# Optimization experiments

Hardware: AMD Instinct MI355X
Metric: run time of the kernel (lower is better)

Reference implementation:

```python
import jax, jax.numpy as jnp
import numpy as np

EPS = 1e-6

def setup_inputs() -> dict:
    key = jax.random.key(0)
    ks = jax.random.split(key, 8)
    B, L, Dm, N, K = 2, 1024, 1024, 64, 4
    Di = Dm * 2  # expand=2
    g = lambda k, shape, scale: jax.random.normal(k, shape, jnp.float32) * scale
    return {
        "x": g(ks[0], (B, L, Dm), 1.0),
        "norm_w": jnp.ones((Dm,), jnp.float32),
        "in_proj_w": g(ks[1], (2 * Di, Dm), 0.02),
        "conv_w": g(ks[2], (Di, 1, K), 0.1),      # depthwise: [out=Di, in/groups=1, K]
        "conv_b": jnp.zeros((Di,), jnp.float32),
        "x_proj_w": g(ks[3], (2 * N, Di), 0.02),
        "dt_w": g(ks[4], (Di, Di), 0.02),
        "dt_b": jnp.ones((Di,), jnp.float32),      # init.constant_(dt_proj.bias, 1.0)
        "A_log": g(ks[5], (Di, N), 1.0) - 4.0,     # normal(mean=-4, std=1)
        "D_param": jnp.ones((Di,), jnp.float32),
        "out_proj_w": g(ks[6], (Dm, Di), 0.02),
    }

def reference(x, norm_w, in_proj_w, conv_w, conv_b, x_proj_w, dt_w, dt_b, A_log, D_param, out_proj_w):
    B, L, Dm = x.shape
    Di = conv_w.shape[0]
    K = conv_w.shape[-1]
    skip = x
    # RMSNorm
    rms = jnp.sqrt(jnp.mean(x * x, axis=-1, keepdims=True) + EPS)
    xn = norm_w * (x / rms)
    # in_proj -> [B,L,2*Di], split into x and res
    xr = xn @ in_proj_w.T
    xi, res = jnp.split(xr, 2, axis=-1)
    # causal depthwise conv1d (pad left K-1, truncate to L == torch pad=K-1 then [:L])
    xc = jax.lax.conv_general_dilated(
        xi.transpose(0, 2, 1), conv_w, window_strides=(1,),
        padding=[(K - 1, 0)], dimension_numbers=("NCH", "OIH", "NCH"),
        feature_group_count=Di)
    xc = (xc + conv_b[None, :, None]).transpose(0, 2, 1)  # [B,L,Di]
    xc = jax.nn.silu(xc)
    # selective scan
    x_dbl = xc @ x_proj_w.T                   # [B,L,2N]; first half (delta) unused, as in source
    _delta, B_ssm = jnp.split(x_dbl, 2, axis=-1)  # B_ssm: [B,L,N]
    dt = jax.nn.softplus(xc @ dt_w.T + dt_b)  # [B,L,Di]
    A = -jnp.exp(A_log.astype(jnp.float32))   # [Di,N]
    N = A.shape[-1]

    def step(h, inp):
        x_t, dt_t, B_t = inp                   # [B,Di],[B,Di],[B,N]
        A_disc = jnp.exp(A[None, :, :] * dt_t[:, :, None])   # [B,Di,N]
        h = A_disc * h + B_t[:, None, :] * x_t[:, :, None]   # [B,Di,N]
        y_t = h.sum(axis=-1) + D_param * x_t                 # [B,Di]
        return h, y_t

    h0 = jnp.zeros((B, Di, N), xc.dtype)
    _, ys = jax.lax.scan(step, h0, (xc.transpose(1, 0, 2), dt.transpose(1, 0, 2), B_ssm.transpose(1, 0, 2)))
    y = ys.transpose(1, 0, 2)                  # [B,L,Di]
    out = (y * jax.nn.silu(res)) @ out_proj_w.T
    return out + skip
```

## Files before the change

kernel.cpp:

```cpp
#include <hip/hip_runtime.h>
#include <hip/hip_bf16.h>
#include <math.h>

#define L_DIM 1024
#define DM 1024
#define DI 2048
#define NS 64

typedef __attribute__((ext_vector_type(8))) short short8;
typedef __attribute__((ext_vector_type(4))) float f32x4;

__device__ __forceinline__ ushort bf16u(float f)
{
    unsigned u = __float_as_uint(f);
    unsigned r = (u + 0x7fffu + ((u >> 16) & 1u)) >> 16;
    return (ushort)r;
}
__device__ __forceinline__ float bf2f(ushort u)
{
    return __uint_as_float((unsigned)u << 16);
}

__device__ __forceinline__ void gld16(const ushort* g, const ushort* l)
{
    __builtin_amdgcn_global_load_lds(
        (const __attribute__((address_space(1))) unsigned int*)g,
        (__attribute__((address_space(3))) unsigned int*)l, 16, 0, 0);
}

__global__ __launch_bounds__(256) void k_rms_xn(const float* __restrict__ x,
    const float* __restrict__ nw, ushort* __restrict__ d)
{
    int row = blockIdx.x;
    const float* xp = x + (size_t)row * DM;
    float4 v = ((const float4*)xp)[threadIdx.x];
    float ss = v.x*v.x + v.y*v.y + v.z*v.z + v.w*v.w;
    #pragma unroll
    for (int m = 32; m; m >>= 1) ss += __shfl_xor(ss, m, 64);
    __shared__ float red[4];
    if ((threadIdx.x & 63) == 0) red[threadIdx.x >> 6] = ss;
    __syncthreads();
    float tot = red[0] + red[1] + red[2] + red[3];
    float ri = rsqrtf(tot * (1.0f / DM) + 1e-6f);
    float4 wv = ((const float4*)nw)[threadIdx.x];
    ((ushort4*)(d + (size_t)row * DM))[threadIdx.x] =
        make_ushort4(bf16u(v.x*ri*wv.x), bf16u(v.y*ri*wv.y),
                     bf16u(v.z*ri*wv.z), bf16u(v.w*ri*wv.w));
}

__device__ __forceinline__ void cast8(const float* __restrict__ s,
                                      ushort* __restrict__ d, int i)
{
    float4 a = ((const float4*)s)[2*i], b = ((const float4*)s)[2*i+1];
    ((ushort4*)d)[2*i]   = make_ushort4(bf16u(a.x), bf16u(a.y), bf16u(a.z), bf16u(a.w));
    ((ushort4*)d)[2*i+1] = make_ushort4(bf16u(b.x), bf16u(b.y), bf16u(b.z), bf16u(b.w));
}
__global__ __launch_bounds__(256) void k_castw(
    const float* __restrict__ s0, ushort* __restrict__ d0,
    const float* __restrict__ s1, ushort* __restrict__ d1,
    const float* __restrict__ s2, ushort* __restrict__ d2,
    const float* __restrict__ s3, ushort* __restrict__ d3)
{
    int i = blockIdx.x * 256 + threadIdx.x;
    if (i < 524288)       cast8(s0, d0, i);
    else if (i < 1048576) cast8(s1, d1, i - 524288);
    else if (i < 1064960) cast8(s2, d2, i - 1048576);
    else                  cast8(s3, d3, i - 1064960);
}

template<int MODE, int BM>
__global__ __launch_bounds__(256) void k_mfma(
    const ushort* __restrict__ Abf, const ushort* __restrict__ Bbf0,
    const ushort* __restrict__ Bbf1, float* __restrict__ C0,
    ushort* __restrict__ C0b, float* __restrict__ C1,
    const float* __restrict__ bias, const float* __restrict__ skip,
    int Kdim, int ldc)
{
    constexpr int NI = (BM == 128) ? 4 : 2;
    constexpr int SA = BM / 32;
    __shared__ __align__(16) ushort As[BM*64];
    __shared__ __align__(16) ushort Bs[128*64];
    const int t = threadIdx.x, w = t >> 6, lane = t & 63;
    const int nwg = gridDim.x * gridDim.y;
    const int orig = blockIdx.y * gridDim.x + blockIdx.x;
    const int swz = (orig & 7) * (nwg >> 3) + (orig >> 3);
    const int nt = swz % gridDim.x, mt = swz / gridDim.x;
    const int mBase = mt * BM, nBase = nt * 128;
    const bool isXP = (MODE == 1) && (nt == 16);
    const ushort* __restrict__ Bbf = isXP ? Bbf1 : Bbf0;
    const int wr = (BM == 128) ? (w >> 1) * 64 : 0;
    const int wc = (BM == 128) ? (w & 1) * 64 : w * 32;
    const int sR = lane >> 3;
    const int sK = ((lane & 7) ^ sR) * 8;

    f32x4 acc[4][NI];
    #pragma unroll
    for (int i = 0; i < 4; ++i)
        #pragma unroll
        for (int j = 0; j < NI; ++j)
            acc[i][j] = (f32x4){0.f, 0.f, 0.f, 0.f};

    for (int kt = 0; kt < Kdim; kt += 64) {
        #pragma unroll
        for (int s = 0; s < SA; ++s) {
            int tr = w*8 + s*32 + sR;
            gld16(Abf + (size_t)(mBase + tr) * Kdim + kt + sK,
                  As + (w*8 + s*32) * 64);
        }
        #pragma unroll
        for (int s = 0; s < 4; ++s) {
            int tr = w*8 + s*32 + sR;
            int gr = isXP ? (tr < 63 ? tr : 63) : (nBase + tr);
            gld16(Bbf + (size_t)gr * Kdim + kt + sK,
                  Bs + (w*8 + s*32) * 64);
        }
        __syncthreads();
        #pragma unroll
        for (int kk = 0; kk < 2; ++kk) {
            short8 af[4], bfr[NI];
            #pragma unroll
            for (int f = 0; f < 4; ++f) {
                int ra = wr + f*16 + (lane & 15);
                int ca = (kk*4 + (lane >> 4)) ^ (ra & 7);
                af[f] = *(const short8*)(As + ra*64 + ca*8);
            }
            #pragma unroll
            for (int f = 0; f < NI; ++f) {
                int rb2 = wc + f*16 + (lane & 15);
                int cb2 = (kk*4 + (lane >> 4)) ^ (rb2 & 7);
                bfr[f] = *(const short8*)(Bs + rb2*64 + cb2*8);
            }
            #pragma unroll
            for (int mi = 0; mi < 4; ++mi)
                #pragma unroll
                for (int ni = 0; ni < NI; ++ni)
                    acc[mi][ni] = __builtin_amdgcn_mfma_f32_16x16x32_bf16(
                        af[mi], bfr[ni], acc[mi][ni], 0, 0, 0);
        }
        __syncthreads();
    }

    const int rb = (lane >> 4) * 4, cbl = lane & 15;
    #pragma unroll
    for (int mi = 0; mi < 4; ++mi) {
        #pragma unroll
        for (int ni = 0; ni < NI; ++ni) {
            int ltcol = wc + ni*16 + cbl;
            int col = nBase + ltcol;
            #pragma unroll
            for (int j = 0; j < 4; ++j) {
                int row = mBase + wr + mi*16 + rb + j;
                float v = acc[mi][ni][j];
                if constexpr (MODE == 0) {
                    C0b[(size_t)row * ldc + col] = bf16u(v);
                } else if constexpr (MODE == 1) {
                    if (isXP) {
                        if (ltcol < NS) C1[(size_t)row * NS + ltcol] = v;
                    } else {
                        float z = v + bias[col];
                        C0[(size_t)row * ldc + col] =
                            (z > 20.f) ? z : logf(1.f + expf(z));
                    }
                } else {
                    C0[(size_t)row * ldc + col] = v + skip[(size_t)row * ldc + col];
                }
            }
        }
    }
}

__global__ __launch_bounds__(256) void k_conv(const ushort* __restrict__ xrb,
    const float* __restrict__ cw, const float* __restrict__ cb,
    float* __restrict__ xc, ushort* __restrict__ xcb)
{
    int gid = blockIdx.x * 256 + threadIdx.x;
    int d = (gid & 511) * 4;
    int tt = (gid >> 9) & 1023;
    int b = gid >> 19;
    float4 w[4];
    #pragma unroll
    for (int c = 0; c < 4; ++c) w[c] = *(const float4*)(cw + (size_t)(d + c) * 4);
    float4 acc = *(const float4*)(cb + d);
    const ushort* base = xrb + (size_t)b * L_DIM * (2*DI) + d;
    #pragma unroll
    for (int j = 0; j < 4; ++j) {
        int ti = tt - 3 + j;
        if (ti < 0) continue;
        ushort4 xu = *(const ushort4*)(base + (size_t)ti * (2*DI));
        const float* w0 = (const float*)&w[0];
        const float* w1 = (const float*)&w[1];
        const float* w2 = (const float*)&w[2];
        const float* w3 = (const float*)&w[3];
        acc.x = fmaf(w0[j], bf2f(xu.x), acc.x);
        acc.y = fmaf(w1[j], bf2f(xu.y), acc.y);
        acc.z = fmaf(w2[j], bf2f(xu.z), acc.z);
        acc.w = fmaf(w3[j], bf2f(xu.w), acc.w);
    }
    acc.x = acc.x / (1.f + expf(-acc.x));
    acc.y = acc.y / (1.f + expf(-acc.y));
    acc.z = acc.z / (1.f + expf(-acc.z));
    acc.w = acc.w / (1.f + expf(-acc.w));
    size_t o = (size_t)(b * L_DIM + tt) * DI + d;
    *(float4*)(xc + o) = acc;
    *(ushort4*)(xcb + o) = make_ushort4(bf16u(acc.x), bf16u(acc.y),
                                        bf16u(acc.z), bf16u(acc.w));
}

__global__ __launch_bounds__(256) void k_tr4(const float* __restrict__ dtb,
    float* __restrict__ dtt, const float* __restrict__ xc,
    float* __restrict__ xct)
{
    __shared__ float tile[64][65];
    const int r0 = blockIdx.y * 64, c0 = blockIdx.x * 64;
    const int z = blockIdx.z;
    const float* s;
    float* d;
    if (z < 2) { s = dtb + (size_t)z * L_DIM * DI;       d = dtt + (size_t)z * DI * L_DIM; }
    else       { s = xc  + (size_t)(z-2) * L_DIM * DI;   d = xct + (size_t)(z-2) * DI * L_DIM; }
    const int tx = threadIdx.x & 15, ty = threadIdx.x >> 4;
    #pragma unroll
    for (int p = 0; p < 4; ++p) {
        float4 v = *(const float4*)(s + (size_t)(r0 + ty + p*16) * DI + c0 + tx*4);
        tile[ty + p*16][tx*4+0] = v.x; tile[ty + p*16][tx*4+1] = v.y;
        tile[ty + p*16][tx*4+2] = v.z; tile[ty + p*16][tx*4+3] = v.w;
    }
    __syncthreads();
    #pragma unroll
    for (int p = 0; p < 4; ++p) {
        int oc = ty + p*16;
        float4 v = make_float4(tile[tx*4+0][oc], tile[tx*4+1][oc],
                               tile[tx*4+2][oc], tile[tx*4+3][oc]);
        *(float4*)(d + (size_t)(c0 + oc) * L_DIM + r0 + tx*4) = v;
    }
}

__global__ __launch_bounds__(256) void k_trg(const float* __restrict__ yt,
    const ushort* __restrict__ xrb, ushort* __restrict__ ybf)
{
    __shared__ float tile[64][65];
    const int r0 = blockIdx.y * 64, c0 = blockIdx.x * 64;
    const int z = blockIdx.z;
    const float* s = yt + (size_t)z * DI * L_DIM;
    const int tx = threadIdx.x & 15, ty = threadIdx.x >> 4;
    #pragma unroll
    for (int p = 0; p < 4; ++p) {
        float4 v = *(const float4*)(s + (size_t)(r0 + ty + p*16) * L_DIM + c0 + tx*4);
        tile[ty + p*16][tx*4+0] = v.x; tile[ty + p*16][tx*4+1] = v.y;
        tile[ty + p*16][tx*4+2] = v.z; tile[ty + p*16][tx*4+3] = v.w;
    }
    __syncthreads();
    #pragma unroll
    for (int p = 0; p < 4; ++p) {
        int oc = ty + p*16;
        int row = z * L_DIM + c0 + oc;
        float4 v = make_float4(tile[tx*4+0][oc], tile[tx*4+1][oc],
                               tile[tx*4+2][oc], tile[tx*4+3][oc]);
        ushort4 gu = *(const ushort4*)(xrb + (size_t)row * (2*DI) + DI + r0 + tx*4);
        float gx = bf2f(gu.x), gy = bf2f(gu.y), gz = bf2f(gu.z), gw = bf2f(gu.w);
        v.x *= gx / (1.f + expf(-gx));
        v.y *= gy / (1.f + expf(-gy));
        v.z *= gz / (1.f + expf(-gz));
        v.w *= gw / (1.f + expf(-gw));
        *(ushort4*)(ybf + (size_t)row * DI + r0 + tx*4) =
            make_ushort4(bf16u(v.x), bf16u(v.y), bf16u(v.z), bf16u(v.w));
    }
}

__device__ __forceinline__ float rl(float v, int lane)
{
    return __int_as_float(__builtin_amdgcn_readlane(__float_as_int(v), lane));
}
__device__ __forceinline__ float exp2_fast(float x)
{
    float r;
    asm("v_exp_f32 %0, %1" : "=v"(r) : "v"(x));
    return r;
}

__global__ __launch_bounds__(256) void k_scan9(const float* __restrict__ dtt,
    const float* __restrict__ xct, const float* __restrict__ Bss,
    const float* __restrict__ A_log, const float* __restrict__ Dp,
    float* __restrict__ yt)
{
    __shared__ float Bsh[64][68];
    __shared__ __align__(16) float Psh[4][64][8];
    const int lane = threadIdx.x & 63;
    const int widx = threadIdx.x >> 6;
    const int b = blockIdx.x >> 9;
    const int d = (blockIdx.x & 511) * 4 + widx;
    const float aL2 = -expf(A_log[(size_t)d * NS + lane]) * 1.44269504f;
    const float Dv = Dp[d];
    const float* dtp = dtt + ((size_t)b * DI + d) * L_DIM;
    const float* xcp = xct + ((size_t)b * DI + d) * L_DIM;
    const float* Bp  = Bss + (size_t)b * L_DIM * NS;
    float* yp = yt + ((size_t)b * DI + d) * L_DIM;
    const int lr = threadIdx.x >> 2;
    const int lc = (threadIdx.x & 3) * 16;
    const int pg = lane >> 3;
    const bool pwrite = (lane & 7) == 7;
    float h = 0.f;

    for (int t0 = 0; t0 < L_DIM; t0 += 64) {
        const float* bsrc = Bp + (size_t)(t0 + lr) * NS + lc;
        float4 b0 = *(const float4*)(bsrc);
        float4 b1 = *(const float4*)(bsrc + 4);
        float4 b2 = *(const float4*)(bsrc + 8);
        float4 b3 = *(const float4*)(bsrc + 12);
        float dt_v = dtp[t0 + lane];
        float xc_v = xcp[t0 + lane];
        __syncthreads();
        *(float4*)&Bsh[lr][lc]      = b0;
        *(float4*)&Bsh[lr][lc + 4]  = b1;
        *(float4*)&Bsh[lr][lc + 8]  = b2;
        *(float4*)&Bsh[lr][lc + 12] = b3;
        __syncthreads();
        #pragma unroll
        for (int q = 0; q < 64; q += 4) {
            float Bv0 = Bsh[q+0][lane];
            float Bv1 = Bsh[q+1][lane];
            float Bv2 = Bsh[q+2][lane];
            float Bv3 = Bsh[q+3][lane];
            float s0, s1, s2, s3;
            {
                float p, ad;
                p  = rl(xc_v, q+0) * Bv0;
                ad = exp2_fast(aL2 * rl(dt_v, q+0));
                h = fmaf(ad, h, p); s0 = h;
                p  = rl(xc_v, q+1) * Bv1;
                ad = exp2_fast(aL2 * rl(dt_v, q+1));
                h = fmaf(ad, h, p); s1 = h;
                p  = rl(xc_v, q+2) * Bv2;
                ad = exp2_fast(aL2 * rl(dt_v, q+2));
                h = fmaf(ad, h, p); s2 = h;
                p  = rl(xc_v, q+3) * Bv3;
                ad = exp2_fast(aL2 * rl(dt_v, q+3));
                h = fmaf(ad, h, p); s3 = h;
            }
            asm("v_add_f32_dpp %0, %0, %0 row_shr:1 row_mask:0xf bank_mask:0xf\n\t"
                "v_add_f32_dpp %1, %1, %1 row_shr:1 row_mask:0xf bank_mask:0xf\n\t"
                "v_add_f32_dpp %2, %2, %2 row_shr:1 row_mask:0xf bank_mask:0xf\n\t"
                "v_add_f32_dpp %3, %3, %3 row_shr:1 row_mask:0xf bank_mask:0xf\n\t"
                "v_add_f32_dpp %0, %0, %0 row_shr:2 row_mask:0xf bank_mask:0xf\n\t"
                "v_add_f32_dpp %1, %1, %1 row_shr:2 row_mask:0xf bank_mask:0xf\n\t"
                "v_add_f32_dpp %2, %2, %2 row_shr:2 row_mask:0xf bank_mask:0xf\n\t"
                "v_add_f32_dpp %3, %3, %3 row_shr:2 row_mask:0xf bank_mask:0xf\n\t"
                "v_add_f32_dpp %0, %0, %0 row_shr:4 row_mask:0xf bank_mask:0xf\n\t"
                "v_add_f32_dpp %1, %1, %1 row_shr:4 row_mask:0xf bank_mask:0xf\n\t"
                "v_add_f32_dpp %2, %2, %2 row_shr:4 row_mask:0xf bank_mask:0xf\n\t"
                "v_add_f32_dpp %3, %3, %3 row_shr:4 row_mask:0xf bank_mask:0xf"
                : "+v"(s0), "+v"(s1), "+v"(s2), "+v"(s3));
            if (pwrite) {
                Psh[widx][q+0][pg] = s0;
                Psh[widx][q+1][pg] = s1;
                Psh[widx][q+2][pg] = s2;
                Psh[widx][q+3][pg] = s3;
            }
        }
        asm volatile("s_waitcnt lgkmcnt(0)" ::: "memory");
        __builtin_amdgcn_sched_barrier(0);
        float4 p0 = *(const float4*)&Psh[widx][lane][0];
        float4 p1 = *(const float4*)&Psh[widx][lane][4];
        float sum = ((p0.x + p0.y) + (p0.z + p0.w))
                  + ((p1.x + p1.y) + (p1.z + p1.w));
        yp[t0 + lane] = fmaf(Dv, xc_v, sum);
    }
}

extern "C" void kernel_launch(void* const* d_in, const int* in_sizes, int n_in,
                              void* d_out, int out_size, void* d_ws, size_t ws_size,
                              hipStream_t stream)
{
    const float* x        = (const float*)d_in[0];
    const float* norm_w   = (const float*)d_in[1];
    const float* in_projw = (const float*)d_in[2];
    const float* conv_w   = (const float*)d_in[3];
    const float* conv_b   = (const float*)d_in[4];
    const float* x_projw  = (const float*)d_in[5];
    const float* dt_w     = (const float*)d_in[6];
    const float* dt_b     = (const float*)d_in[7];
    const float* A_log    = (const float*)d_in[8];
    const float* D_param  = (const float*)d_in[9];
    const float* out_projw= (const float*)d_in[10];
    float* out = (float*)d_out;

    float* ws = (float*)d_ws;
    ushort* xr_bf = (ushort*)ws;
    float* xc   = ws + (size_t)4*1024*1024;
    float* dtb  = xc + (size_t)4*1024*1024;
    float* Bss  = dtb + (size_t)4*1024*1024;
    float* dtt  = Bss + 131072;
    float* xct  = dtt + (size_t)4*1024*1024;
    ushort* xn_bf  = (ushort*)(xct + (size_t)4*1024*1024);
    ushort* xc_bf  = xn_bf + (size_t)2*1024*1024;
    ushort* xpw_bf = xc_bf + (size_t)4*1024*1024;
    ushort* opw_bf = xpw_bf + 131072;
    ushort* inpw_bf = (ushort*)dtt;
    ushort* dtw_bf  = (ushort*)xct;
    ushort* y_bf    = (ushort*)xc;
    float* yt = dtb;

    k_castw<<<5184, 256, 0, stream>>>(in_projw, inpw_bf, dt_w, dtw_bf,
                                      x_projw + (size_t)64*2048, xpw_bf,
                                      out_projw, opw_bf);
    k_rms_xn<<<2048, 256, 0, stream>>>(x, norm_w, xn_bf);
    k_mfma<0,128><<<dim3(32, 16), 256, 0, stream>>>(xn_bf, inpw_bf, nullptr,
                                                nullptr, xr_bf, nullptr,
                                                nullptr, nullptr, 1024, 4096);
    k_conv<<<4096, 256, 0, stream>>>(xr_bf, conv_w, conv_b, xc, xc_bf);
    k_mfma<1,128><<<dim3(17, 16), 256, 0, stream>>>(xc_bf, dtw_bf, xpw_bf,
                                                dtb, nullptr, Bss,
                                                dt_b, nullptr, 2048, 2048);
    k_tr4<<<dim3(32, 16, 4), 256, 0, stream>>>(dtb, dtt, xc, xct);
    k_scan9<<<1024, 256, 0, stream>>>(dtt, xct, Bss, A_log, D_param, yt);
    k_trg<<<dim3(16, 32, 2), 256, 0, stream>>>(yt, xr_bf, y_bf);
    k_mfma<2,64><<<dim3(8, 32), 256, 0, stream>>>(y_bf, opw_bf, nullptr,
                                               out, nullptr, nullptr,
                                               nullptr, x, 2048, 1024);
}
```

Baseline: 259.5 us.

## Store dt, conv output and scan output as bf16 intermediates

Softplus dt, the conv output and the scan output are now stored as bf16 instead of fp32. The fp32 copy of the conv output is dropped, and the transpose and gate kernels are rewritten to move 16-byte bf16 vectors through an XOR-swizzled shared tile. The workspace layout is reorganised to match. This roughly halves the memory traffic of the transposes and the scan inputs and outputs, at the cost of bf16 rounding on dt, x and y that feeds the exponential scan recurrence.

```diff
diff --git a/kernel.cpp b/kernel.cpp
--- a/kernel.cpp
+++ b/kernel.cpp
@@ -158,8 +158,8 @@
                         if (ltcol < NS) C1[(size_t)row * NS + ltcol] = v;
                     } else {
                         float z = v + bias[col];
-                        C0[(size_t)row * ldc + col] =
-                            (z > 20.f) ? z : logf(1.f + expf(z));
+                        float sp = (z > 20.f) ? z : logf(1.f + expf(z));
+                        C0b[(size_t)row * ldc + col] = bf16u(sp);
                     }
                 } else {
                     C0[(size_t)row * ldc + col] = v + skip[(size_t)row * ldc + col];
@@ -171,7 +171,7 @@
 
 __global__ __launch_bounds__(256) void k_conv(const ushort* __restrict__ xrb,
     const float* __restrict__ cw, const float* __restrict__ cb,
-    float* __restrict__ xc, ushort* __restrict__ xcb)
+    ushort* __restrict__ xcb)
 {
     int gid = blockIdx.x * 256 + threadIdx.x;
     int d = (gid & 511) * 4;
@@ -201,68 +201,73 @@
     acc.z = acc.z / (1.f + expf(-acc.z));
     acc.w = acc.w / (1.f + expf(-acc.w));
     size_t o = (size_t)(b * L_DIM + tt) * DI + d;
-    *(float4*)(xc + o) = acc;
     *(ushort4*)(xcb + o) = make_ushort4(bf16u(acc.x), bf16u(acc.y),
                                         bf16u(acc.z), bf16u(acc.w));
 }
 
-__global__ __launch_bounds__(256) void k_tr4(const float* __restrict__ dtb,
-    float* __restrict__ dtt, const float* __restrict__ xc,
-    float* __restrict__ xct)
-{
-    __shared__ float tile[64][65];
+__global__ __launch_bounds__(256) void k_tr4(const ushort* __restrict__ dtb,
+    ushort* __restrict__ dtt, const ushort* __restrict__ xcb,
+    ushort* __restrict__ xct)
+{
+    __shared__ __align__(16) ushort tile[64][72];
     const int r0 = blockIdx.y * 64, c0 = blockIdx.x * 64;
     const int z = blockIdx.z;
-    const float* s;
-    float* d;
+    const ushort* s;
+    ushort* d;
     if (z < 2) { s = dtb + (size_t)z * L_DIM * DI;       d = dtt + (size_t)z * DI * L_DIM; }
-    else       { s = xc  + (size_t)(z-2) * L_DIM * DI;   d = xct + (size_t)(z-2) * DI * L_DIM; }
-    const int tx = threadIdx.x & 15, ty = threadIdx.x >> 4;
-    #pragma unroll
-    for (int p = 0; p < 4; ++p) {
-        float4 v = *(const float4*)(s + (size_t)(r0 + ty + p*16) * DI + c0 + tx*4);
-        tile[ty + p*16][tx*4+0] = v.x; tile[ty + p*16][tx*4+1] = v.y;
-        tile[ty + p*16][tx*4+2] = v.z; tile[ty + p*16][tx*4+3] = v.w;
+    else       { s = xcb + (size_t)(z-2) * L_DIM * DI;   d = xct + (size_t)(z-2) * DI * L_DIM; }
+    const int tx = threadIdx.x & 7, ty = threadIdx.x >> 3;
+    #pragma unroll
+    for (int p = 0; p < 2; ++p) {
+        int r = ty + p*32;
+        short8 v = *(const short8*)(s + (size_t)(r0 + r) * DI + c0 + tx*8);
+        int g = tx ^ ((r >> 3) & 7);
+        *(short8*)&tile[r][g*8] = v;
     }
     __syncthreads();
     #pragma unroll
-    for (int p = 0; p < 4; ++p) {
-        int oc = ty + p*16;
-        float4 v = make_float4(tile[tx*4+0][oc], tile[tx*4+1][oc],
-                               tile[tx*4+2][oc], tile[tx*4+3][oc]);
-        *(float4*)(d + (size_t)(c0 + oc) * L_DIM + r0 + tx*4) = v;
-    }
-}
-
-__global__ __launch_bounds__(256) void k_trg(const float* __restrict__ yt,
+    for (int p = 0; p < 2; ++p) {
+        int crow = ty + p*32;
+        ushort o[8];
+        #pragma unroll
+        for (int j = 0; j < 8; ++j)
+            o[j] = tile[tx*8 + j][(((crow >> 3) ^ tx) << 3) + (crow & 7)];
+        *(short8*)(d + (size_t)(c0 + crow) * L_DIM + r0 + tx*8) = *(short8*)o;
+    }
+}
+
+__global__ __launch_bounds__(256) void k_trg(const ushort* __restrict__ yt,
     const ushort* __restrict__ xrb, ushort* __restrict__ ybf)
 {
-    __shared__ float tile[64][65];
+    __shared__ __align__(16) ushort tile[64][72];
     const int r0 = blockIdx.y * 64, c0 = blockIdx.x * 64;
     const int z = blockIdx.z;
-    const float* s = yt + (size_t)z * DI * L_DIM;
-    const int tx = threadIdx.x & 15, ty = threadIdx.x >> 4;
-    #pragma unroll
-    for (int p = 0; p < 4; ++p) {
-        float4 v = *(const float4*)(s + (size_t)(r0 + ty + p*16) * L_DIM + c0 + tx*4);
-        tile[ty + p*16][tx*4+0] = v.x; tile[ty + p*16][tx*4+1] = v.y;
-        tile[ty + p*16][tx*4+2] = v.z; tile[ty + p*16][tx*4+3] = v.w;
+    const ushort* s = yt + (size_t)z * DI * L_DIM;
+    const int tx = threadIdx.x & 7, ty = threadIdx.x >> 3;
+    #pragma unroll
+    for (int p = 0; p < 2; ++p) {
+        int r = ty + p*32;
+        short8 v = *(const short8*)(s + (size_t)(r0 + r) * L_DIM + c0 + tx*8);
+        int g = tx ^ ((r >> 3) & 7);
+        *(short8*)&tile[r][g*8] = v;
     }
     __syncthreads();
     #pragma unroll
-    for (int p = 0; p < 4; ++p) {
-        int oc = ty + p*16;
-        int row = z * L_DIM + c0 + oc;
-        float4 v = make_float4(tile[tx*4+0][oc], tile[tx*4+1][oc],
-                               tile[tx*4+2][oc], tile[tx*4+3][oc]);
-        ushort4 gu = *(const ushort4*)(xrb + (size_t)row * (2*DI) + DI + r0 + tx*4);
-        float gx = bf2f(gu.x), gy = bf2f(gu.y), gz = bf2f(gu.z), gw = bf2f(gu.w);
-        v.x *= gx / (1.f + expf(-gx));
-        v.y *= gy / (1.f + expf(-gy));
-        v.z *= gz / (1.f + expf(-gz));
-        v.w *= gw / (1.f + expf(-gw));
-        *(ushort4*)(ybf + (size_t)row * DI + r0 + tx*4) =
-            make_ushort4(bf16u(v.x), bf16u(v.y), bf16u(v.z), bf16u(v.w));
+    for (int p = 0; p < 2; ++p) {
+        int crow = ty + p*32;
+        int row = z * L_DIM + c0 + crow;
+        ushort4 gu0 = *(const ushort4*)(xrb + (size_t)row * (2*DI) + DI + r0 + tx*8);
+        ushort4 gu1 = *(const ushort4*)(xrb + (size_t)row * (2*DI) + DI + r0 + tx*8 + 4);
+        ushort o[8];
+        const ushort* gp = (const ushort*)&gu0;
+        #pragma unroll
+        for (int j = 0; j < 8; ++j) {
+            float yv = bf2f(tile[tx*8 + j][(((crow >> 3) ^ tx) << 3) + (crow & 7)]);
+            float g = bf2f(j < 4 ? ((const ushort*)&gu0)[j] : ((const ushort*)&gu1)[j-4]);
+            o[j] = bf16u(yv * g / (1.f + expf(-g)));
+        }
+        (void)gp;
+        *(short8*)(ybf + (size_t)row * DI + r0 + tx*8) = *(short8*)o;
     }
 }
 
@@ -277,10 +282,10 @@
     return r;
 }
 
-__global__ __launch_bounds__(256) void k_scan9(const float* __restrict__ dtt,
-    const float* __restrict__ xct, const float* __restrict__ Bss,
+__global__ __launch_bounds__(256) void k_scan9(const ushort* __restrict__ dtt,
+    const ushort* __restrict__ xct, const float* __restrict__ Bss,
     const float* __restrict__ A_log, const float* __restrict__ Dp,
-    float* __restrict__ yt)
+    ushort* __restrict__ yt)
 {
     __shared__ float Bsh[64][68];
     __shared__ __align__(16) float Psh[4][64][8];
@@ -290,10 +295,10 @@
     const int d = (blockIdx.x & 511) * 4 + widx;
     const float aL2 = -expf(A_log[(size_t)d * NS + lane]) * 1.44269504f;
     const float Dv = Dp[d];
-    const float* dtp = dtt + ((size_t)b * DI + d) * L_DIM;
-    const float* xcp = xct + ((size_t)b * DI + d) * L_DIM;
+    const ushort* dtp = dtt + ((size_t)b * DI + d) * L_DIM;
+    const ushort* xcp = xct + ((size_t)b * DI + d) * L_DIM;
     const float* Bp  = Bss + (size_t)b * L_DIM * NS;
-    float* yp = yt + ((size_t)b * DI + d) * L_DIM;
+    ushort* yp = yt + ((size_t)b * DI + d) * L_DIM;
     const int lr = threadIdx.x >> 2;
     const int lc = (threadIdx.x & 3) * 16;
     const int pg = lane >> 3;
@@ -306,8 +311,8 @@
         float4 b1 = *(const float4*)(bsrc + 4);
         float4 b2 = *(const float4*)(bsrc + 8);
         float4 b3 = *(const float4*)(bsrc + 12);
-        float dt_v = dtp[t0 + lane];
-        float xc_v = xcp[t0 + lane];
+        float dt_v = bf2f(dtp[t0 + lane]);
+        float xc_v = bf2f(xcp[t0 + lane]);
         __syncthreads();
         *(float4*)&Bsh[lr][lc]      = b0;
         *(float4*)&Bsh[lr][lc + 4]  = b1;
@@ -362,7 +367,7 @@
         float4 p1 = *(const float4*)&Psh[widx][lane][4];
         float sum = ((p0.x + p0.y) + (p0.z + p0.w))
                   + ((p1.x + p1.y) + (p1.z + p1.w));
-        yp[t0 + lane] = fmaf(Dv, xc_v, sum);
+        yp[t0 + lane] = bf16u(fmaf(Dv, xc_v, sum));
     }
 }
 
@@ -383,21 +388,20 @@
     const float* out_projw= (const float*)d_in[10];
     float* out = (float*)d_out;
 
-    float* ws = (float*)d_ws;
-    ushort* xr_bf = (ushort*)ws;
-    float* xc   = ws + (size_t)4*1024*1024;
-    float* dtb  = xc + (size_t)4*1024*1024;
-    float* Bss  = dtb + (size_t)4*1024*1024;
-    float* dtt  = Bss + 131072;
-    float* xct  = dtt + (size_t)4*1024*1024;
-    ushort* xn_bf  = (ushort*)(xct + (size_t)4*1024*1024);
-    ushort* xc_bf  = xn_bf + (size_t)2*1024*1024;
-    ushort* xpw_bf = xc_bf + (size_t)4*1024*1024;
+    ushort* wsu = (ushort*)d_ws;
+    ushort* xr_bf  = wsu;
+    ushort* xc_bf  = xr_bf + (size_t)8*1024*1024;
+    ushort* dtb_bf = xc_bf + (size_t)4*1024*1024;
+    ushort* dtt_bf = dtb_bf + (size_t)4*1024*1024;
+    ushort* xct_bf = dtt_bf + (size_t)4*1024*1024;
+    ushort* xn_bf  = xct_bf + (size_t)4*1024*1024;
+    ushort* xpw_bf = xn_bf + (size_t)2*1024*1024;
     ushort* opw_bf = xpw_bf + 131072;
-    ushort* inpw_bf = (ushort*)dtt;
-    ushort* dtw_bf  = (ushort*)xct;
-    ushort* y_bf    = (ushort*)xc;
-    float* yt = dtb;
+    float*  Bss    = (float*)(opw_bf + (size_t)2*1024*1024);
+    ushort* inpw_bf = dtt_bf;
+    ushort* dtw_bf  = xct_bf;
+    ushort* y_bf    = xc_bf;
+    ushort* yt_bf   = dtb_bf;
 
     k_castw<<<5184, 256, 0, stream>>>(in_projw, inpw_bf, dt_w, dtw_bf,
                                       x_projw + (size_t)64*2048, xpw_bf,
@@ -406,13 +410,13 @@
     k_mfma<0,128><<<dim3(32, 16), 256, 0, stream>>>(xn_bf, inpw_bf, nullptr,
                                                 nullptr, xr_bf, nullptr,
                                                 nullptr, nullptr, 1024, 4096);
-    k_conv<<<4096, 256, 0, stream>>>(xr_bf, conv_w, conv_b, xc, xc_bf);
+    k_conv<<<4096, 256, 0, stream>>>(xr_bf, conv_w, conv_b, xc_bf);
     k_mfma<1,128><<<dim3(17, 16), 256, 0, stream>>>(xc_bf, dtw_bf, xpw_bf,
-                                                dtb, nullptr, Bss,
+                                                nullptr, dtb_bf, Bss,
                                                 dt_b, nullptr, 2048, 2048);
-    k_tr4<<<dim3(32, 16, 4), 256, 0, stream>>>(dtb, dtt, xc, xct);
-    k_scan9<<<1024, 256, 0, stream>>>(dtt, xct, Bss, A_log, D_param, yt);
-    k_trg<<<dim3(16, 32, 2), 256, 0, stream>>>(yt, xr_bf, y_bf);
+    k_tr4<<<dim3(32, 16, 4), 256, 0, stream>>>(dtb_bf, dtt_bf, xc_bf, xct_bf);
+    k_scan9<<<1024, 256, 0, stream>>>(dtt_bf, xct_bf, Bss, A_log, D_param, yt_bf);
+    k_trg<<<dim3(16, 32, 2), 256, 0, stream>>>(yt_bf, xr_bf, y_bf);
     k_mfma<2,64><<<dim3(8, 32), 256, 0, stream>>>(y_bf, opw_bf, nullptr,
                                                out, nullptr, nullptr,
                                                nullptr, x, 2048, 1024);
```

After: 253.9 us. -2.2%, faster.
